# Kernel optimization log

Measured on AMD Instinct MI355X. Metric: run time of the kernel, lower is better.

## Reference

```python
import jax, jax.numpy as jnp
import numpy as np

D_MODEL = 64     # input_dim // 4
D_INNER = 128    # expand * d_model
D_STATE = 16
D_CONV = 4
DT_RANK = 4      # ceil(d_model / 16)
EPS = 1e-5


def layernorm(x, g, b):
    m = x.mean(-1, keepdims=True)
    v = x.var(-1, keepdims=True)
    return (x - m) * jax.lax.rsqrt(v + EPS) * g + b


def mamba(u, W_in, W_conv, b_conv, W_xproj, W_dt, b_dt, A_log, Dp, W_out):
    # u: [B, L, d_model]
    B, L, _ = u.shape
    xz = u @ W_in.T                              # [B, L, 2*d_inner]
    xi, z = xz[..., :D_INNER], xz[..., D_INNER:]
    # depthwise causal conv1d over L
    xp = jnp.pad(xi, ((0, 0), (D_CONV - 1, 0), (0, 0)))
    xc = b_conv + sum(xp[:, k:k + L, :] * W_conv[:, k] for k in range(D_CONV))
    xc = jax.nn.silu(xc)                         # [B, L, d_inner]
    proj = xc @ W_xproj.T                        # [B, L, dt_rank + 2*d_state]
    dtp = proj[..., :DT_RANK]
    Bm = proj[..., DT_RANK:DT_RANK + D_STATE]    # [B, L, d_state]
    Cm = proj[..., DT_RANK + D_STATE:]           # [B, L, d_state]
    dt = jax.nn.softplus(dtp @ W_dt.T + b_dt)    # [B, L, d_inner]
    A = -jnp.exp(A_log)                          # [d_inner, d_state]
    dA = jnp.exp(dt[..., None] * A)              # [B, L, d_inner, d_state]
    dBx = (dt * xc)[..., None] * Bm[:, :, None, :]

    def step(h, t):
        dA_t, dBx_t, C_t = t
        h = dA_t * h + dBx_t                     # [B, d_inner, d_state]
        return h, jnp.einsum('bds,bs->bd', h, C_t)

    h0 = jnp.zeros((B, D_INNER, D_STATE), u.dtype)
    _, ys = jax.lax.scan(step, h0, (dA.transpose(1, 0, 2, 3),
                                    dBx.transpose(1, 0, 2, 3),
                                    Cm.transpose(1, 0, 2)))
    y = ys.transpose(1, 0, 2) + Dp * xc          # [B, L, d_inner]
    y = y * jax.nn.silu(z)
    return y @ W_out.T                           # [B, L, d_model]


def _forward(x, x1, x2, x3, g1, be1, g2, be2, g3, be3, g4, be4, skip_scale,
             W_in, W_conv, b_conv, W_xproj, W_dt, b_dt, A_log, D, W_out):
    Bb, C = x.shape[:2]
    img_dims = x2.shape[2:]
    mparams = (W_in, W_conv, b_conv, W_xproj, W_dt, b_dt, A_log, D, W_out)

    def branch(inp, g, b):
        xf = inp.reshape(Bb, C, -1).transpose(0, 2, 1)   # [B, L, C]
        xn = layernorm(xf, g, b)
        return mamba(xn, *mparams) + skip_scale * xn

    x_mamba = jnp.concatenate([branch(x, g1, be1), branch(x1, g2, be2),
                               branch(x2, g3, be3), branch(x3, g4, be4)], axis=2)
    out = x_mamba.transpose(0, 2, 1).reshape(Bb, 4 * C, *img_dims)
    return out


def setup_inputs():
    key = jax.random.key(0)
    ks = jax.random.split(key, 12)
    f = lambda k, shp, s=1.0: jax.random.normal(k, shp, dtype=jnp.float32) * s
    inp = {
        'x': f(ks[0], (8, 64, 32, 32)),
        'x1': f(ks[1], (8, 64, 32, 32)),
        'x2': f(ks[2], (8, 64, 32, 32)),
        'x3': f(ks[3], (8, 64, 32, 32)),
        'g1': jnp.ones(64), 'be1': jnp.zeros(64),
        'g2': jnp.ones(64), 'be2': jnp.zeros(64),
        'g3': jnp.ones(64), 'be3': jnp.zeros(64),
        'g4': jnp.ones(64), 'be4': jnp.zeros(64),
        'skip_scale': jnp.ones((1,), jnp.float32),
        'W_in': f(ks[4], (2 * D_INNER, D_MODEL), 0.1),
        'W_conv': f(ks[5], (D_INNER, D_CONV), 0.3),
        'b_conv': jnp.zeros(D_INNER),
        'W_xproj': f(ks[6], (DT_RANK + 2 * D_STATE, D_INNER), 0.1),
        'W_dt': f(ks[7], (D_INNER, DT_RANK), 0.1),
        'b_dt': f(ks[8], (D_INNER,), 0.1),
        'A_log': jnp.log(jnp.tile(jnp.arange(1, D_STATE + 1, dtype=jnp.float32), (D_INNER, 1))),
        'D': jnp.ones(D_INNER),
        'W_out': f(ks[9], (D_MODEL, D_INNER), 0.1),
    }
    return inp


def reference(x, x1, x2, x3, g1, be1, g2, be2, g3, be3, g4, be4, skip_scale,
              W_in, W_conv, b_conv, W_xproj, W_dt, b_dt, A_log, D, W_out):
    return _forward(x, x1, x2, x3, g1, be1, g2, be2, g3, be3, g4, be4, skip_scale,
                    W_in, W_conv, b_conv, W_xproj, W_dt, b_dt, A_log, D, W_out)
```

## Files before the change

### kernel.cpp

```cpp
#include <hip/hip_runtime.h>
#include <hip/hip_bf16.h>

#define L2E 1.4426950408889634f
#define LN2 0.6931471805599453f

__device__ __forceinline__ float fexp2(float x) { return __builtin_amdgcn_exp2f(x); }
__device__ __forceinline__ float flog2(float x) { return __builtin_amdgcn_logf(x); }
__device__ __forceinline__ int uniform(int x) { return __builtin_amdgcn_readfirstlane(x); }
__device__ __forceinline__ float sigmoidf_(float v) { return 1.f / (1.f + fexp2(-v * L2E)); }
__device__ __forceinline__ float softplusf_(float t) {
    return (t > 20.f) ? t : LN2 * flog2(1.f + fexp2(t * L2E));
}

constexpr size_t O_M   = 0;
constexpr size_t O_RS  = 32768;
constexpr size_t O_G   = 65536;
constexpr size_t O_Z   = 4259840;
constexpr size_t O_XC  = 8454144;
constexpr size_t O_BM  = 12648448;
constexpr size_t O_CM  = 13172736;
constexpr size_t O_DTP = 13697024;
constexpr size_t O_HP  = 13828096;
constexpr size_t O_DT  = 18022400;
constexpr size_t O_DX  = 22216704;

__global__ __launch_bounds__(256) void k1_ln_inproj(
    const float* __restrict__ x0, const float* __restrict__ x1,
    const float* __restrict__ x2, const float* __restrict__ x3,
    const float* __restrict__ win,
    const float* __restrict__ g1, const float* __restrict__ be1,
    const float* __restrict__ g2, const float* __restrict__ be2,
    const float* __restrict__ g3, const float* __restrict__ be3,
    const float* __restrict__ g4, const float* __restrict__ be4,
    float* __restrict__ ws)
{
    __shared__ float sX[64 * 68];
    __shared__ float sW[64 * 68];
    __shared__ float sM[64], sR[64];
    int bid = blockIdx.x;
    int seq = bid >> 6, jb = (bid >> 4) & 3, pb = bid & 15;
    int branch = seq >> 3, b = seq & 7;
    int tid = threadIdx.x;
    int lane = tid & 63;
    int wq = uniform(tid >> 6);
    const float* xin = (branch==0)?x0:(branch==1)?x1:(branch==2)?x2:x3;
    const float* gam = (branch==0)?g1:(branch==1)?g2:(branch==2)?g3:g4;
    const float* bet = (branch==0)?be1:(branch==1)?be2:(branch==2)?be3:be4;
    const float* xb = xin + (size_t)b * 65536;

#pragma unroll
    for (int r = 0; r < 16; ++r) {
        int row = r * 4 + wq;
        sX[row * 68 + lane] = xb[(size_t)row * 1024 + pb * 64 + lane];
        sW[lane * 68 + row] = win[(size_t)(jb * 64 + row) * 64 + lane];
    }
    __syncthreads();
    if (tid < 64) {
        float sum = 0.f, sq = 0.f;
#pragma unroll
        for (int c = 0; c < 64; ++c) {
            float v = sX[c * 68 + tid];
            sum += v; sq += v * v;
        }
        float mean = sum * (1.f/64.f);
        float var  = sq * (1.f/64.f) - mean * mean;
        float rs   = rsqrtf(var + 1e-5f);
        sM[tid] = mean; sR[tid] = rs;
        if (jb == 0) {
            ws[O_M  + (size_t)seq * 1024 + pb * 64 + tid] = mean;
            ws[O_RS + (size_t)seq * 1024 + pb * 64 + tid] = rs;
        }
    }
    __syncthreads();
#pragma unroll
    for (int r = 0; r < 16; ++r) {
        int c = r * 4 + wq;
        float v = sX[c * 68 + lane];
        sX[c * 68 + lane] = (v - sM[lane]) * sR[lane] * gam[c] + bet[c];
    }
    __syncthreads();
    int jt = tid >> 4, pt = tid & 15;
    float acc[4][4];
#pragma unroll
    for (int i = 0; i < 4; ++i)
#pragma unroll
        for (int j = 0; j < 4; ++j) acc[i][j] = 0.f;
    for (int c = 0; c < 64; ++c) {
        float4 wv = *(const float4*)&sW[c * 68 + jt * 4];
        float4 xv = *(const float4*)&sX[c * 68 + pt * 4];
        float w[4] = {wv.x, wv.y, wv.z, wv.w};
        float x[4] = {xv.x, xv.y, xv.z, xv.w};
#pragma unroll
        for (int i = 0; i < 4; ++i)
#pragma unroll
            for (int j = 0; j < 4; ++j) acc[i][j] += w[i] * x[j];
    }
    int p0 = pb * 64 + pt * 4;
    float* xi = ws + O_G + (size_t)seq * 131072;
    float* zz = ws + O_Z + (size_t)seq * 131072;
#pragma unroll
    for (int ji = 0; ji < 4; ++ji) {
        int j = jb * 64 + jt * 4 + ji;
        float4 v = make_float4(acc[ji][0], acc[ji][1], acc[ji][2], acc[ji][3]);
        if (j < 128) *(float4*)&xi[(size_t)j * 1024 + p0] = v;
        else         *(float4*)&zz[(size_t)(j - 128) * 1024 + p0] = v;
    }
}

__global__ __launch_bounds__(256) void k2_conv_proj(
    const float* __restrict__ wconv, const float* __restrict__ bconv,
    const float* __restrict__ wxp,
    const float* __restrict__ wdt, const float* __restrict__ bdt,
    float* __restrict__ ws)
{
    __shared__ float sX[128 * 68];
    __shared__ float sWr[4 * 128 * 12];
    __shared__ __align__(16) float sDtp4[64 * 4];
    int bid = blockIdx.x;
    int seq = bid >> 4, ptile = bid & 15;
    int tid = threadIdx.x;
    int lane = tid & 63;
    int wq = uniform(tid >> 6);
    int p0 = ptile * 64;
    int p  = p0 + lane;
    int j0 = wq * 9;

    const float* xirow = ws + O_G  + (size_t)seq * 131072;
    float*       xcrow = ws + O_XC + (size_t)seq * 131072;

#pragma unroll 4
    for (int r = 0; r < 32; ++r) {
        int d = r * 4 + wq;
        const float* row = xirow + (size_t)d * 1024;
        int gp = p0 - 3 + lane;
        sX[d * 68 + lane] = (gp >= 0) ? row[gp] : 0.f;
        if (lane < 3) sX[d * 68 + 64 + lane] = row[p0 + 61 + lane];
    }
#pragma unroll
    for (int jj = 0; jj < 9; ++jj) {
#pragma unroll
        for (int half = 0; half < 2; ++half) {
            int d = half * 64 + lane;
            sWr[(wq * 128 + d) * 12 + jj] = wxp[(size_t)(j0 + jj) * 128 + d];
        }
    }
    __syncthreads();

#pragma unroll 2
    for (int dd = 0; dd < 32; ++dd) {
        int d = wq * 32 + dd;
        float4 wc = *(const float4*)&wconv[d * 4];
        float v = bconv[d];
        float* rowl = &sX[d * 68];
        v += rowl[lane + 0] * wc.x;
        v += rowl[lane + 1] * wc.y;
        v += rowl[lane + 2] * wc.z;
        v += rowl[lane + 3] * wc.w;
        v = v * sigmoidf_(v);
        xcrow[(size_t)d * 1024 + p] = v;
        rowl[lane + 3] = v;
    }
    __syncthreads();

    float acc[9];
#pragma unroll
    for (int jj = 0; jj < 9; ++jj) acc[jj] = 0.f;
#pragma unroll 4
    for (int d = 0; d < 128; ++d) {
        float xcv = sX[d * 68 + 3 + lane];
        const float* wr = &sWr[(wq * 128 + d) * 12];
        float4 wA = *(const float4*)wr;
        float4 wB = *(const float4*)(wr + 4);
        float  w8 = wr[8];
        acc[0] += wA.x * xcv; acc[1] += wA.y * xcv;
        acc[2] += wA.z * xcv; acc[3] += wA.w * xcv;
        acc[4] += wB.x * xcv; acc[5] += wB.y * xcv;
        acc[6] += wB.z * xcv; acc[7] += wB.w * xcv;
        acc[8] += w8 * xcv;
    }

    float* Bm = ws + O_BM + (size_t)seq * 16384;
    float* Cm = ws + O_CM + (size_t)seq * 16384;
#pragma unroll
    for (int jj = 0; jj < 9; ++jj) {
        int j = j0 + jj;
        if (j < 4) continue;
        float t = acc[jj];
        if (j < 20) Bm[(size_t)(j - 4)  * 1024 + p] = t;
        else        Cm[(size_t)(j - 20) * 1024 + p] = t;
    }

    if (wq == 0)
        *(float4*)&sDtp4[lane * 4] = make_float4(acc[0], acc[1], acc[2], acc[3]);
    __syncthreads();
    float* dtg = ws + O_DT + (size_t)seq * 131072;
    float* dxg = ws + O_DX + (size_t)seq * 131072;
    float4 qv = *(const float4*)&sDtp4[lane * 4];
#pragma unroll 4
    for (int dd = 0; dd < 32; ++dd) {
        int d = wq * 32 + dd;
        float4 wv = *(const float4*)&wdt[d * 4];
        float t = bdt[d] + qv.x*wv.x + qv.y*wv.y + qv.z*wv.z + qv.w*wv.w;
        float dt = softplusf_(t);
        float dx = dt * sX[d * 68 + 3 + lane];
        dtg[(size_t)d * 1024 + p] = dt;
        dxg[(size_t)d * 1024 + p] = dx;
    }
}

__device__ __forceinline__ void a2_preload(const float* alog, int d0, int s0, float* a2)
{
    float4 a0 = *(const float4*)(alog + d0 * 16 + s0);
    float4 a1 = *(const float4*)(alog + (d0 + 1) * 16 + s0);
    a2[0] = -fexp2(a0.x * L2E) * L2E; a2[1] = -fexp2(a0.y * L2E) * L2E;
    a2[2] = -fexp2(a0.z * L2E) * L2E; a2[3] = -fexp2(a0.w * L2E) * L2E;
    a2[4] = -fexp2(a1.x * L2E) * L2E; a2[5] = -fexp2(a1.y * L2E) * L2E;
    a2[6] = -fexp2(a1.z * L2E) * L2E; a2[7] = -fexp2(a1.w * L2E) * L2E;
}

__global__ __launch_bounds__(256) void k3a_scan(const float* __restrict__ alog,
                                                float* __restrict__ ws)
{
    __shared__ __align__(16) float sB[32 * 16];
    int bid = blockIdx.x;
    int seq = bid >> 5, ch = bid & 31;
    int lb = ch * 32;
    int tid = threadIdx.x;
    int d0 = (tid >> 2) * 2, s0 = (tid & 3) * 4;

    float a2[8];
    a2_preload(alog, d0, s0, a2);

    const float* Bmg = ws + O_BM + (size_t)seq * 16384;
    for (int i = tid; i < 512; i += 256) {
        int s = i >> 5, li = i & 31;
        sB[li * 16 + s] = Bmg[(size_t)s * 1024 + lb + li];
    }
    __syncthreads();

    const float* r0t = ws + O_DT + (size_t)seq * 131072 + (size_t)d0 * 1024 + lb;
    const float* r1t = r0t + 1024;
    const float* r0x = ws + O_DX + (size_t)seq * 131072 + (size_t)d0 * 1024 + lb;
    const float* r1x = r0x + 1024;

    float h[8];
#pragma unroll
    for (int i = 0; i < 8; ++i) h[i] = 0.f;
    float sdt0 = 0.f, sdt1 = 0.f;
    for (int q4 = 0; q4 < 8; ++q4) {
        float4 t0 = *(const float4*)&r0t[q4 * 4];
        float4 t1 = *(const float4*)&r1t[q4 * 4];
        float4 x0 = *(const float4*)&r0x[q4 * 4];
        float4 x1 = *(const float4*)&r1x[q4 * 4];
        float t0a[4] = {t0.x, t0.y, t0.z, t0.w};
        float t1a[4] = {t1.x, t1.y, t1.z, t1.w};
        float x0a[4] = {x0.x, x0.y, x0.z, x0.w};
        float x1a[4] = {x1.x, x1.y, x1.z, x1.w};
#pragma unroll
        for (int k = 0; k < 4; ++k) {
            int li = q4 * 4 + k;
            float dt0 = t0a[k], dt1 = t1a[k];
            float dx0 = x0a[k], dx1 = x1a[k];
            float4 Bv = *(const float4*)&sB[li * 16 + s0];
            float bv[4] = {Bv.x, Bv.y, Bv.z, Bv.w};
            sdt0 += dt0; sdt1 += dt1;
#pragma unroll
            for (int ss = 0; ss < 4; ++ss) {
                float e0 = fexp2(dt0 * a2[ss]);
                h[ss] = e0 * h[ss] + dx0 * bv[ss];
                float e1 = fexp2(dt1 * a2[4 + ss]);
                h[4 + ss] = e1 * h[4 + ss] + dx1 * bv[ss];
            }
        }
    }
    float* hp = ws + O_HP + (size_t)(seq * 32 + ch) * 4096;
#pragma unroll
    for (int ss = 0; ss < 4; ++ss) {
        hp[d0 * 16 + s0 + ss]              = fexp2(a2[ss] * sdt0);
        hp[(d0 + 1) * 16 + s0 + ss]        = fexp2(a2[4 + ss] * sdt1);
        hp[2048 + d0 * 16 + s0 + ss]       = h[ss];
        hp[2048 + (d0 + 1) * 16 + s0 + ss] = h[4 + ss];
    }
}

__global__ __launch_bounds__(256) void k3b_compose(float* __restrict__ ws)
{
    int seq = blockIdx.x >> 3, dg = blockIdx.x & 7;
    int idx = dg * 256 + threadIdx.x;
    float h = 0.f;
    float* hpb = ws + O_HP + (size_t)seq * 32 * 4096;
    float P = hpb[idx];
    float E = hpb[2048 + idx];
    for (int c = 0; c < 32; ++c) {
        float* hp = hpb + (size_t)c * 4096;
        float Pn = 0.f, En = 0.f;
        if (c < 31) { Pn = hp[4096 + idx]; En = hp[4096 + 2048 + idx]; }
        hp[idx] = h;
        h = P * h + E;
        P = Pn; E = En;
    }
}

__global__ __launch_bounds__(256) void k3cd(
    const float* __restrict__ alog,
    const float* __restrict__ x0, const float* __restrict__ x1,
    const float* __restrict__ x2, const float* __restrict__ x3,
    const float* __restrict__ g1, const float* __restrict__ be1,
    const float* __restrict__ g2, const float* __restrict__ be2,
    const float* __restrict__ g3, const float* __restrict__ be3,
    const float* __restrict__ g4, const float* __restrict__ be4,
    const float* __restrict__ dpar, const float* __restrict__ woutp,
    const float* __restrict__ skipp, float* __restrict__ ws,
    float* __restrict__ out)
{
    __shared__ __align__(16) float sY[128 * 36];
    __shared__ __align__(16) float sB[32 * 16];
    __shared__ __align__(16) float sC[32 * 16];
    int bid = blockIdx.x;
    int seq = bid >> 5, ch = bid & 31;
    int branch = seq >> 3, b = seq & 7;
    int lb = ch * 32;
    int tid = threadIdx.x;
    int sq = tid & 3;
    int d0 = (tid >> 2) * 2, s0 = sq * 4;

    float a2[8];
    a2_preload(alog, d0, s0, a2);

    const float* Bmg = ws + O_BM + (size_t)seq * 16384;
    const float* Cmg = ws + O_CM + (size_t)seq * 16384;
    for (int i = tid; i < 512; i += 256) {
        int s = i >> 5, li = i & 31;
        sB[li * 16 + s] = Bmg[(size_t)s * 1024 + lb + li];
        sC[li * 16 + s] = Cmg[(size_t)s * 1024 + lb + li];
    }

    const float* hp = ws + O_HP + (size_t)(seq * 32 + ch) * 4096;
    float4 H0 = *(const float4*)&hp[d0 * 16 + s0];
    float4 H1 = *(const float4*)&hp[(d0 + 1) * 16 + s0];
    float h[8] = {H0.x, H0.y, H0.z, H0.w, H1.x, H1.y, H1.z, H1.w};
    __syncthreads();

    const float* r0t = ws + O_DT + (size_t)seq * 131072 + (size_t)d0 * 1024 + lb;
    const float* r1t = r0t + 1024;
    const float* r0x = ws + O_DX + (size_t)seq * 131072 + (size_t)d0 * 1024 + lb;
    const float* r1x = r0x + 1024;

    for (int q4 = 0; q4 < 8; ++q4) {
        float4 t0 = *(const float4*)&r0t[q4 * 4];
        float4 t1 = *(const float4*)&r1t[q4 * 4];
        float4 x0v = *(const float4*)&r0x[q4 * 4];
        float4 x1v = *(const float4*)&r1x[q4 * 4];
        float t0a[4] = {t0.x, t0.y, t0.z, t0.w};
        float t1a[4] = {t1.x, t1.y, t1.z, t1.w};
        float x0a[4] = {x0v.x, x0v.y, x0v.z, x0v.w};
        float x1a[4] = {x1v.x, x1v.y, x1v.z, x1v.w};
#pragma unroll
        for (int k = 0; k < 4; ++k) {
            int li = q4 * 4 + k;
            float dt0 = t0a[k], dt1 = t1a[k];
            float dx0 = x0a[k], dx1 = x1a[k];
            float4 Bv = *(const float4*)&sB[li * 16 + s0];
            float4 Cv = *(const float4*)&sC[li * 16 + s0];
            float bv[4] = {Bv.x, Bv.y, Bv.z, Bv.w};
            float cv[4] = {Cv.x, Cv.y, Cv.z, Cv.w};
            float acc0 = 0.f, acc1 = 0.f;
#pragma unroll
            for (int ss = 0; ss < 4; ++ss) {
                float e0 = fexp2(dt0 * a2[ss]);
                h[ss] = e0 * h[ss] + dx0 * bv[ss];
                acc0 += h[ss] * cv[ss];
                float e1 = fexp2(dt1 * a2[4 + ss]);
                h[4 + ss] = e1 * h[4 + ss] + dx1 * bv[ss];
                acc1 += h[4 + ss] * cv[ss];
            }
            acc0 += __shfl_xor(acc0, 1); acc0 += __shfl_xor(acc0, 2);
            acc1 += __shfl_xor(acc1, 1); acc1 += __shfl_xor(acc1, 2);
            if (sq == 0) {
                sY[d0 * 36 + li]       = acc0;
                sY[(d0 + 1) * 36 + li] = acc1;
            }
        }
    }
    __syncthreads();

    const float* zzg = ws + O_Z  + (size_t)seq * 131072;
    const float* xcg = ws + O_XC + (size_t)seq * 131072;
    for (int i = tid; i < 4096; i += 256) {
        int d = i >> 5, li = i & 31;
        float zv  = zzg[(size_t)d * 1024 + lb + li];
        float xcv = xcg[(size_t)d * 1024 + lb + li];
        float yv  = sY[d * 36 + li];
        sY[d * 36 + li] = (yv + dpar[d] * xcv) * (zv * sigmoidf_(zv));
    }
    __syncthreads();

    int ctt = tid >> 3;
    int ptq = tid & 7;
    int c0 = ctt * 2;
    const float* w0p = woutp + (size_t)c0 * 128;
    const float* w1p = w0p + 128;
    float acc[2][4];
#pragma unroll
    for (int i = 0; i < 2; ++i)
#pragma unroll
        for (int j = 0; j < 4; ++j) acc[i][j] = 0.f;
    for (int d4 = 0; d4 < 32; ++d4) {
        float4 wa = *(const float4*)&w0p[d4 * 4];
        float4 wb = *(const float4*)&w1p[d4 * 4];
        float waa[4] = {wa.x, wa.y, wa.z, wa.w};
        float wba[4] = {wb.x, wb.y, wb.z, wb.w};
#pragma unroll
        for (int k = 0; k < 4; ++k) {
            int d = d4 * 4 + k;
            float4 gv = *(const float4*)&sY[d * 36 + ptq * 4];
            acc[0][0] += waa[k] * gv.x; acc[0][1] += waa[k] * gv.y;
            acc[0][2] += waa[k] * gv.z; acc[0][3] += waa[k] * gv.w;
            acc[1][0] += wba[k] * gv.x; acc[1][1] += wba[k] * gv.y;
            acc[1][2] += wba[k] * gv.z; acc[1][3] += wba[k] * gv.w;
        }
    }

    const float* xin = (branch==0)?x0:(branch==1)?x1:(branch==2)?x2:x3;
    const float* gam = (branch==0)?g1:(branch==1)?g2:(branch==2)?g3:g4;
    const float* bet = (branch==0)?be1:(branch==1)?be2:(branch==2)?be3:be4;
    const float* xb = xin + (size_t)b * 65536;
    int pp = lb + ptq * 4;
    float skipv = skipp[0];
    float4 m4 = *(const float4*)&ws[O_M  + (size_t)seq * 1024 + pp];
    float4 r4 = *(const float4*)&ws[O_RS + (size_t)seq * 1024 + pp];
    float mm[4] = {m4.x, m4.y, m4.z, m4.w};
    float rr[4] = {r4.x, r4.y, r4.z, r4.w};
#pragma unroll
    for (int ci = 0; ci < 2; ++ci) {
        int c = c0 + ci;
        float4 xv = *(const float4*)&xb[(size_t)c * 1024 + pp];
        float xvv[4] = {xv.x, xv.y, xv.z, xv.w};
        float gc = gam[c], bc = bet[c];
        float o[4];
#pragma unroll
        for (int pi = 0; pi < 4; ++pi) {
            float xn = (xvv[pi] - mm[pi]) * rr[pi] * gc + bc;
            o[pi] = acc[ci][pi] + skipv * xn;
        }
        *(float4*)&out[((size_t)b * 256 + branch * 64 + c) * 1024 + pp] =
            make_float4(o[0], o[1], o[2], o[3]);
    }
}

extern "C" void kernel_launch(void* const* d_in, const int* in_sizes, int n_in,
                              void* d_out, int out_size, void* d_ws, size_t ws_size,
                              hipStream_t stream) {
    float* ws = (float*)d_ws;
    auto f = [&](int i) { return (const float*)d_in[i]; };
    hipLaunchKernelGGL(k1_ln_inproj, dim3(2048), dim3(256), 0, stream,
        f(0), f(1), f(2), f(3), f(13),
        f(4), f(5), f(6), f(7), f(8), f(9), f(10), f(11), ws);
    hipLaunchKernelGGL(k2_conv_proj, dim3(512), dim3(256), 0, stream,
        f(14), f(15), f(16), f(17), f(18), ws);
    hipLaunchKernelGGL(k3a_scan, dim3(1024), dim3(256), 0, stream, f(19), ws);
    hipLaunchKernelGGL(k3b_compose, dim3(256), dim3(256), 0, stream, ws);
    hipLaunchKernelGGL(k3cd, dim3(1024), dim3(256), 0, stream,
        f(19),
        f(0), f(1), f(2), f(3),
        f(4), f(5), f(6), f(7), f(8), f(9), f(10), f(11),
        f(20), f(21), f(12), ws, (float*)d_out);
}
```

Measured before the change: 214.1 us.

## Fuse chunk scan into conv/proj kernel and loop in_proj column blocks per block

The per-chunk selective-scan pass (k3a) is folded into the conv/x_proj kernel, which now keeps dt, dt*x and B in shared memory and writes the chunk decay products and partial states directly, removing one launch and the re-read of dt/dx/B from global memory. The LN+in_proj kernel now handles all four output column blocks in one block by looping over weight tiles, so the layernorm of each input tile is computed once instead of four times. The cost is fewer blocks (512 instead of 2048 and 1024), which lowers parallelism and occupancy, plus extra shared memory and more serial work per block.

```diff
diff --git a/kernel.cpp b/kernel.cpp
--- a/kernel.cpp
+++ b/kernel.cpp
@@ -19,7 +19,6 @@
 constexpr size_t O_XC  = 8454144;
 constexpr size_t O_BM  = 12648448;
 constexpr size_t O_CM  = 13172736;
-constexpr size_t O_DTP = 13697024;
 constexpr size_t O_HP  = 13828096;
 constexpr size_t O_DT  = 18022400;
 constexpr size_t O_DX  = 22216704;
@@ -38,7 +37,7 @@
     __shared__ float sW[64 * 68];
     __shared__ float sM[64], sR[64];
     int bid = blockIdx.x;
-    int seq = bid >> 6, jb = (bid >> 4) & 3, pb = bid & 15;
+    int seq = bid >> 4, pb = bid & 15;
     int branch = seq >> 3, b = seq & 7;
     int tid = threadIdx.x;
     int lane = tid & 63;
@@ -52,7 +51,6 @@
     for (int r = 0; r < 16; ++r) {
         int row = r * 4 + wq;
         sX[row * 68 + lane] = xb[(size_t)row * 1024 + pb * 64 + lane];
-        sW[lane * 68 + row] = win[(size_t)(jb * 64 + row) * 64 + lane];
     }
     __syncthreads();
     if (tid < 64) {
@@ -66,10 +64,8 @@
         float var  = sq * (1.f/64.f) - mean * mean;
         float rs   = rsqrtf(var + 1e-5f);
         sM[tid] = mean; sR[tid] = rs;
-        if (jb == 0) {
-            ws[O_M  + (size_t)seq * 1024 + pb * 64 + tid] = mean;
-            ws[O_RS + (size_t)seq * 1024 + pb * 64 + tid] = rs;
-        }
+        ws[O_M  + (size_t)seq * 1024 + pb * 64 + tid] = mean;
+        ws[O_RS + (size_t)seq * 1024 + pb * 64 + tid] = rs;
     }
     __syncthreads();
 #pragma unroll
@@ -79,31 +75,42 @@
         sX[c * 68 + lane] = (v - sM[lane]) * sR[lane] * gam[c] + bet[c];
     }
     __syncthreads();
+
     int jt = tid >> 4, pt = tid & 15;
-    float acc[4][4];
-#pragma unroll
-    for (int i = 0; i < 4; ++i)
-#pragma unroll
-        for (int j = 0; j < 4; ++j) acc[i][j] = 0.f;
-    for (int c = 0; c < 64; ++c) {
-        float4 wv = *(const float4*)&sW[c * 68 + jt * 4];
-        float4 xv = *(const float4*)&sX[c * 68 + pt * 4];
-        float w[4] = {wv.x, wv.y, wv.z, wv.w};
-        float x[4] = {xv.x, xv.y, xv.z, xv.w};
-#pragma unroll
-        for (int i = 0; i < 4; ++i)
-#pragma unroll
-            for (int j = 0; j < 4; ++j) acc[i][j] += w[i] * x[j];
-    }
     int p0 = pb * 64 + pt * 4;
     float* xi = ws + O_G + (size_t)seq * 131072;
     float* zz = ws + O_Z + (size_t)seq * 131072;
-#pragma unroll
-    for (int ji = 0; ji < 4; ++ji) {
-        int j = jb * 64 + jt * 4 + ji;
-        float4 v = make_float4(acc[ji][0], acc[ji][1], acc[ji][2], acc[ji][3]);
-        if (j < 128) *(float4*)&xi[(size_t)j * 1024 + p0] = v;
-        else         *(float4*)&zz[(size_t)(j - 128) * 1024 + p0] = v;
+
+    for (int jb = 0; jb < 4; ++jb) {
+#pragma unroll
+        for (int r = 0; r < 16; ++r) {
+            int row = r * 4 + wq;
+            sW[lane * 68 + row] = win[(size_t)(jb * 64 + row) * 64 + lane];
+        }
+        __syncthreads();
+        float acc[4][4];
+#pragma unroll
+        for (int i = 0; i < 4; ++i)
+#pragma unroll
+            for (int j = 0; j < 4; ++j) acc[i][j] = 0.f;
+        for (int c = 0; c < 64; ++c) {
+            float4 wv = *(const float4*)&sW[c * 68 + jt * 4];
+            float4 xv = *(const float4*)&sX[c * 68 + pt * 4];
+            float w[4] = {wv.x, wv.y, wv.z, wv.w};
+            float x[4] = {xv.x, xv.y, xv.z, xv.w};
+#pragma unroll
+            for (int i = 0; i < 4; ++i)
+#pragma unroll
+                for (int j = 0; j < 4; ++j) acc[i][j] += w[i] * x[j];
+        }
+#pragma unroll
+        for (int ji = 0; ji < 4; ++ji) {
+            int j = jb * 64 + jt * 4 + ji;
+            float4 v = make_float4(acc[ji][0], acc[ji][1], acc[ji][2], acc[ji][3]);
+            if (j < 128) *(float4*)&xi[(size_t)j * 1024 + p0] = v;
+            else         *(float4*)&zz[(size_t)(j - 128) * 1024 + p0] = v;
+        }
+        __syncthreads();
     }
 }
 
@@ -111,11 +118,16 @@
     const float* __restrict__ wconv, const float* __restrict__ bconv,
     const float* __restrict__ wxp,
     const float* __restrict__ wdt, const float* __restrict__ bdt,
+    const float* __restrict__ alog,
     float* __restrict__ ws)
 {
-    __shared__ float sX[128 * 68];
-    __shared__ float sWr[4 * 128 * 12];
+    __shared__ float buf[17408];
     __shared__ __align__(16) float sDtp4[64 * 4];
+    __shared__ float sB5[64 * 20];
+    float* sX  = buf;
+    float* sWr = buf + 8704;
+    float* sDt = buf + 8704;
+
     int bid = blockIdx.x;
     int seq = bid >> 4, ptile = bid & 15;
     int tid = threadIdx.x;
@@ -186,13 +198,13 @@
         int j = j0 + jj;
         if (j < 4) continue;
         float t = acc[jj];
-        if (j < 20) Bm[(size_t)(j - 4)  * 1024 + p] = t;
+        if (j < 20) { Bm[(size_t)(j - 4) * 1024 + p] = t; sB5[lane * 20 + (j - 4)] = t; }
         else        Cm[(size_t)(j - 20) * 1024 + p] = t;
     }
-
     if (wq == 0)
         *(float4*)&sDtp4[lane * 4] = make_float4(acc[0], acc[1], acc[2], acc[3]);
     __syncthreads();
+
     float* dtg = ws + O_DT + (size_t)seq * 131072;
     float* dxg = ws + O_DX + (size_t)seq * 131072;
     float4 qv = *(const float4*)&sDtp4[lane * 4];
@@ -202,9 +214,75 @@
         float4 wv = *(const float4*)&wdt[d * 4];
         float t = bdt[d] + qv.x*wv.x + qv.y*wv.y + qv.z*wv.z + qv.w*wv.w;
         float dt = softplusf_(t);
-        float dx = dt * sX[d * 68 + 3 + lane];
+        float xc = sX[d * 68 + 3 + lane];
+        float dx = dt * xc;
         dtg[(size_t)d * 1024 + p] = dt;
         dxg[(size_t)d * 1024 + p] = dx;
+        sDt[d * 68 + lane] = dt;
+        sX [d * 68 + lane] = dx;
+    }
+    __syncthreads();
+
+    {
+        int dA = tid >> 2;
+        int dB = dA + 64;
+        int s05 = (tid & 3) * 4;
+        float a2[8];
+        {
+            float4 a0 = *(const float4*)(alog + dA * 16 + s05);
+            float4 a1 = *(const float4*)(alog + dB * 16 + s05);
+            a2[0] = -fexp2(a0.x * L2E) * L2E; a2[1] = -fexp2(a0.y * L2E) * L2E;
+            a2[2] = -fexp2(a0.z * L2E) * L2E; a2[3] = -fexp2(a0.w * L2E) * L2E;
+            a2[4] = -fexp2(a1.x * L2E) * L2E; a2[5] = -fexp2(a1.y * L2E) * L2E;
+            a2[6] = -fexp2(a1.z * L2E) * L2E; a2[7] = -fexp2(a1.w * L2E) * L2E;
+        }
+        float* hp0 = ws + O_HP + (size_t)(seq * 32 + ptile * 2) * 4096;
+#pragma unroll
+        for (int cc = 0; cc < 2; ++cc) {
+            const float* dtA = &sDt[dA * 68 + cc * 32];
+            const float* dtB = &sDt[dB * 68 + cc * 32];
+            const float* dxA = &sX [dA * 68 + cc * 32];
+            const float* dxB = &sX [dB * 68 + cc * 32];
+            float h[8];
+#pragma unroll
+            for (int i = 0; i < 8; ++i) h[i] = 0.f;
+            float sdtA = 0.f, sdtB = 0.f;
+            for (int q4 = 0; q4 < 8; ++q4) {
+                float4 t0 = *(const float4*)&dtA[q4 * 4];
+                float4 t1 = *(const float4*)&dtB[q4 * 4];
+                float4 x0 = *(const float4*)&dxA[q4 * 4];
+                float4 x1 = *(const float4*)&dxB[q4 * 4];
+                float t0a[4] = {t0.x, t0.y, t0.z, t0.w};
+                float t1a[4] = {t1.x, t1.y, t1.z, t1.w};
+                float x0a[4] = {x0.x, x0.y, x0.z, x0.w};
+                float x1a[4] = {x1.x, x1.y, x1.z, x1.w};
+#pragma unroll
+                for (int k = 0; k < 4; ++k) {
+                    int li = q4 * 4 + k;
+                    float4 Bv = *(const float4*)&sB5[(cc * 32 + li) * 20 + s05];
+                    float bv[4] = {Bv.x, Bv.y, Bv.z, Bv.w};
+                    float dt0 = t0a[k], dt1 = t1a[k];
+                    float dx0 = x0a[k], dx1 = x1a[k];
+                    sdtA += dt0; sdtB += dt1;
+#pragma unroll
+                    for (int ss = 0; ss < 4; ++ss) {
+                        float e0 = fexp2(dt0 * a2[ss]);
+                        h[ss] = e0 * h[ss] + dx0 * bv[ss];
+                        float e1 = fexp2(dt1 * a2[4 + ss]);
+                        h[4 + ss] = e1 * h[4 + ss] + dx1 * bv[ss];
+                    }
+                }
+            }
+            float* hp = hp0 + cc * 4096;
+            *(float4*)&hp[dA * 16 + s05] = make_float4(
+                fexp2(a2[0] * sdtA), fexp2(a2[1] * sdtA),
+                fexp2(a2[2] * sdtA), fexp2(a2[3] * sdtA));
+            *(float4*)&hp[dB * 16 + s05] = make_float4(
+                fexp2(a2[4] * sdtB), fexp2(a2[5] * sdtB),
+                fexp2(a2[6] * sdtB), fexp2(a2[7] * sdtB));
+            *(float4*)&hp[2048 + dA * 16 + s05] = make_float4(h[0], h[1], h[2], h[3]);
+            *(float4*)&hp[2048 + dB * 16 + s05] = make_float4(h[4], h[5], h[6], h[7]);
+        }
     }
 }
 
@@ -216,71 +294,6 @@
     a2[2] = -fexp2(a0.z * L2E) * L2E; a2[3] = -fexp2(a0.w * L2E) * L2E;
     a2[4] = -fexp2(a1.x * L2E) * L2E; a2[5] = -fexp2(a1.y * L2E) * L2E;
     a2[6] = -fexp2(a1.z * L2E) * L2E; a2[7] = -fexp2(a1.w * L2E) * L2E;
-}
-
-__global__ __launch_bounds__(256) void k3a_scan(const float* __restrict__ alog,
-                                                float* __restrict__ ws)
-{
-    __shared__ __align__(16) float sB[32 * 16];
-    int bid = blockIdx.x;
-    int seq = bid >> 5, ch = bid & 31;
-    int lb = ch * 32;
-    int tid = threadIdx.x;
-    int d0 = (tid >> 2) * 2, s0 = (tid & 3) * 4;
-
-    float a2[8];
-    a2_preload(alog, d0, s0, a2);
-
-    const float* Bmg = ws + O_BM + (size_t)seq * 16384;
-    for (int i = tid; i < 512; i += 256) {
-        int s = i >> 5, li = i & 31;
-        sB[li * 16 + s] = Bmg[(size_t)s * 1024 + lb + li];
-    }
-    __syncthreads();
-
-    const float* r0t = ws + O_DT + (size_t)seq * 131072 + (size_t)d0 * 1024 + lb;
-    const float* r1t = r0t + 1024;
-    const float* r0x = ws + O_DX + (size_t)seq * 131072 + (size_t)d0 * 1024 + lb;
-    const float* r1x = r0x + 1024;
-
-    float h[8];
-#pragma unroll
-    for (int i = 0; i < 8; ++i) h[i] = 0.f;
-    float sdt0 = 0.f, sdt1 = 0.f;
-    for (int q4 = 0; q4 < 8; ++q4) {
-        float4 t0 = *(const float4*)&r0t[q4 * 4];
-        float4 t1 = *(const float4*)&r1t[q4 * 4];
-        float4 x0 = *(const float4*)&r0x[q4 * 4];
-        float4 x1 = *(const float4*)&r1x[q4 * 4];
-        float t0a[4] = {t0.x, t0.y, t0.z, t0.w};
-        float t1a[4] = {t1.x, t1.y, t1.z, t1.w};
-        float x0a[4] = {x0.x, x0.y, x0.z, x0.w};
-        float x1a[4] = {x1.x, x1.y, x1.z, x1.w};
-#pragma unroll
-        for (int k = 0; k < 4; ++k) {
-            int li = q4 * 4 + k;
-            float dt0 = t0a[k], dt1 = t1a[k];
-            float dx0 = x0a[k], dx1 = x1a[k];
-            float4 Bv = *(const float4*)&sB[li * 16 + s0];
-            float bv[4] = {Bv.x, Bv.y, Bv.z, Bv.w};
-            sdt0 += dt0; sdt1 += dt1;
-#pragma unroll
-            for (int ss = 0; ss < 4; ++ss) {
-                float e0 = fexp2(dt0 * a2[ss]);
-                h[ss] = e0 * h[ss] + dx0 * bv[ss];
-                float e1 = fexp2(dt1 * a2[4 + ss]);
-                h[4 + ss] = e1 * h[4 + ss] + dx1 * bv[ss];
-            }
-        }
-    }
-    float* hp = ws + O_HP + (size_t)(seq * 32 + ch) * 4096;
-#pragma unroll
-    for (int ss = 0; ss < 4; ++ss) {
-        hp[d0 * 16 + s0 + ss]              = fexp2(a2[ss] * sdt0);
-        hp[(d0 + 1) * 16 + s0 + ss]        = fexp2(a2[4 + ss] * sdt1);
-        hp[2048 + d0 * 16 + s0 + ss]       = h[ss];
-        hp[2048 + (d0 + 1) * 16 + s0 + ss] = h[4 + ss];
-    }
 }
 
 __global__ __launch_bounds__(256) void k3b_compose(float* __restrict__ ws)
@@ -453,12 +466,11 @@
                               hipStream_t stream) {
     float* ws = (float*)d_ws;
     auto f = [&](int i) { return (const float*)d_in[i]; };
-    hipLaunchKernelGGL(k1_ln_inproj, dim3(2048), dim3(256), 0, stream,
+    hipLaunchKernelGGL(k1_ln_inproj, dim3(512), dim3(256), 0, stream,
         f(0), f(1), f(2), f(3), f(13),
         f(4), f(5), f(6), f(7), f(8), f(9), f(10), f(11), ws);
     hipLaunchKernelGGL(k2_conv_proj, dim3(512), dim3(256), 0, stream,
-        f(14), f(15), f(16), f(17), f(18), ws);
-    hipLaunchKernelGGL(k3a_scan, dim3(1024), dim3(256), 0, stream, f(19), ws);
+        f(14), f(15), f(16), f(17), f(18), f(19), ws);
     hipLaunchKernelGGL(k3b_compose, dim3(256), dim3(256), 0, stream, ws);
     hipLaunchKernelGGL(k3cd, dim3(1024), dim3(256), 0, stream,
         f(19),
```

Measured after the change: 203.5 us. 1.05x faster.
